# Kernel tuning notes

Hardware: AMD Instinct MI355X
Metric: run time of the kernel (lower is better)

Reference implementation:

```python
import jax, jax.numpy as jnp
import numpy as np

EPS = 1e-10
B, S, D, K = 8, 2048, 512, 1024
TEMP = 1.0  # quantizer temperature set to 1.0 in SQVAE.__init__


def _ln(x, g, b):
    m = x.mean(-1, keepdims=True)
    v = x.var(-1, keepdims=True)
    return (x - m) / jnp.sqrt(v + 1e-5) * g + b


def _mlp(x, w1, b1, g1, be1, w2, b2, g2, be2):
    # feed_forward: Linear -> ReLU -> LayerNorm, twice (MLPLayers=2)
    h = _ln(jax.nn.relu(x @ w1 + b1), g1, be1)
    return _ln(jax.nn.relu(h @ w2 + b2), g2, be2)


def setup_inputs() -> dict:
    key = jax.random.key(0)
    ks = jax.random.split(key, 20)
    W = 0.04  # small init scale to keep distances / softmax well-conditioned
    p = lambda k, sh, s=1.0: jax.random.normal(k, sh, dtype=jnp.float32) * s
    return {
        'x': p(ks[0], (B, S, D)),
        'gumbel_u': jax.random.uniform(ks[1], (B * S, K), dtype=jnp.float32),
        'enc_w1': p(ks[2], (D, D), W), 'enc_b1': jnp.zeros(D, jnp.float32),
        'enc_g1': jnp.ones(D, jnp.float32), 'enc_be1': jnp.zeros(D, jnp.float32),
        'enc_w2': p(ks[3], (D, D), W), 'enc_b2': jnp.zeros(D, jnp.float32),
        'enc_g2': jnp.ones(D, jnp.float32), 'enc_be2': jnp.zeros(D, jnp.float32),
        'dec_w1': p(ks[4], (D, D), W), 'dec_b1': jnp.zeros(D, jnp.float32),
        'dec_g1': jnp.ones(D, jnp.float32), 'dec_be1': jnp.zeros(D, jnp.float32),
        'dec_w2': p(ks[5], (D, D), W), 'dec_b2': jnp.zeros(D, jnp.float32),
        'dec_g2': jnp.ones(D, jnp.float32), 'dec_be2': jnp.zeros(D, jnp.float32),
        'codebook': p(ks[6], (K, D)),
        'log_param_q': jnp.zeros((), jnp.float32),
    }


def reference(x, gumbel_u, enc_w1, enc_b1, enc_g1, enc_be1, enc_w2, enc_b2, enc_g2, enc_be2,
              dec_w1, dec_b1, dec_g1, dec_be1, dec_w2, dec_b2, dec_g2, dec_be2,
              codebook, log_param_q):
    bs, seq, d = x.shape
    z = _mlp(x, enc_w1, enc_b1, enc_g1, enc_be1, enc_w2, enc_b2, enc_g2, enc_be2)
    # gaussian_1: log_var_q = 0 -> var_q = exp(log_param_q_scalar)
    var_q = jnp.exp(log_param_q)
    w = 0.5 / jnp.clip(var_q, 1e-10)  # 0.5 * precision_q (scalar)
    zf = z.reshape(-1, d)  # [N, D]
    # cdist^2 style distance, scaled by weight -> logits [N, K]
    dist = w * (jnp.sum(zf * zf, axis=1, keepdims=True)
                + jnp.sum(codebook * codebook, axis=1)
                - 2.0 * zf @ codebook.T)
    logit = -dist
    logp = jax.nn.log_softmax(logit, axis=-1)
    probs = jnp.exp(logp)
    # gumbel-softmax sample (train path), noise provided as uniform input
    g = -jnp.log(-jnp.log(gumbel_u + EPS) + EPS)
    encodings = jax.nn.softmax((logit + g) / TEMP, axis=-1)
    z_q = (encodings @ codebook).reshape(bs, seq, d)
    kld_discrete = jnp.sum(probs * logp) / bs
    kld_continuous = jnp.mean(jnp.sum((z - z_q) ** 2 * w, axis=(1, 2)))
    loss = kld_discrete + kld_continuous
    avg_probs = jnp.mean(jax.lax.stop_gradient(probs), axis=0)
    perplexity = jnp.exp(-jnp.sum(avg_probs * jnp.log(avg_probs + 1e-7)))
    x_rec = _mlp(z_q, dec_w1, dec_b1, dec_g1, dec_be1, dec_w2, dec_b2, dec_g2, dec_be2)
    return x_rec, loss, perplexity
```

## Files before the change

### kernel.cpp

```cpp
#include <hip/hip_runtime.h>
#include <math.h>

#define NROWS 16384
#define DIM   512
#define KCODE 1024

typedef __attribute__((ext_vector_type(8))) __bf16 bf16x8;
typedef __attribute__((ext_vector_type(4))) float f32x4;

__device__ __forceinline__ float wave_reduce_sum(float v) {
  #pragma unroll
  for (int m = 1; m < 64; m <<= 1) v += __shfl_xor(v, m, 64);
  return v;
}
__device__ __forceinline__ float wave_reduce_max(float v) {
  #pragma unroll
  for (int m = 1; m < 64; m <<= 1) v = fmaxf(v, __shfl_xor(v, m, 64));
  return v;
}
__device__ __forceinline__ unsigned short f2bf(float f) {
  union { float f; unsigned u; } v; v.f = f;
  unsigned r = v.u + 0x7FFFu + ((v.u >> 16) & 1u);
  return (unsigned short)(r >> 16);
}
__device__ __forceinline__ float bf2f(unsigned short h) {
  union { unsigned u; float f; } v; v.u = ((unsigned)h) << 16;
  return v.f;
}
__device__ __forceinline__ uint4 pack8(const float* x) {
  uint4 r;
  r.x = (unsigned)f2bf(x[0]) | ((unsigned)f2bf(x[1]) << 16);
  r.y = (unsigned)f2bf(x[2]) | ((unsigned)f2bf(x[3]) << 16);
  r.z = (unsigned)f2bf(x[4]) | ((unsigned)f2bf(x[5]) << 16);
  r.w = (unsigned)f2bf(x[6]) | ((unsigned)f2bf(x[7]) << 16);
  return r;
}

__device__ __forceinline__ void glds16(const void* g, void* lds) {
  __builtin_amdgcn_global_load_lds(
      (const __attribute__((address_space(1))) unsigned int*)g,
      (__attribute__((address_space(3))) unsigned int*)lds, 16, 0, 0);
}

__global__ __launch_bounds__(512, 2) void dist_fused(
    const unsigned short* __restrict__ zhp, const unsigned short* __restrict__ zlp,
    const unsigned short* __restrict__ cbh, const unsigned short* __restrict__ cbl,
    const float* __restrict__ znorm, const float* __restrict__ cnorm,
    const float* __restrict__ lpq, float* __restrict__ outf) {
  __shared__ char smem[131072];
  const int t = threadIdx.x;
  const int l = t & 63, w = t >> 6;
  const int wm = w >> 2, wn = w & 3;
  const int b = blockIdx.x;
  const int xcd = b & 7, j = b >> 3;
  const int m0 = (xcd * 8 + j / 4) * 256;
  const int n0 = (j % 4) * 256;

  f32x4 acc[8][4];
  #pragma unroll
  for (int i = 0; i < 8; ++i)
    #pragma unroll
    for (int jj = 0; jj < 4; ++jj) acc[i][jj] = (f32x4){0.f, 0.f, 0.f, 0.f};

  const int row = l & 15;
  const int kcol = (l >> 4) * 8;
  const size_t aLo = (size_t)(m0 + w * 16 + row) * 512 + kcol;
  const size_t aHi = aLo + (size_t)128 * 512;
  const size_t bLo = (size_t)(n0 + w * 16 + row) * 512 + kcol;
  const size_t bHi = bLo + (size_t)128 * 512;

  auto issue = [&](int s) {
    char* hb = smem + (s & 1) * 65536;
    const int kt = s * 32;
    glds16(zhp + aLo + kt, hb + w * 1024);
    glds16(zhp + aHi + kt, hb + (w + 8) * 1024);
    glds16(zlp + aLo + kt, hb + 16384 + w * 1024);
    glds16(zlp + aHi + kt, hb + 16384 + (w + 8) * 1024);
    glds16(cbh + bLo + kt, hb + 32768 + w * 1024);
    glds16(cbh + bHi + kt, hb + 32768 + (w + 8) * 1024);
    glds16(cbl + bLo + kt, hb + 49152 + w * 1024);
    glds16(cbl + bHi + kt, hb + 49152 + (w + 8) * 1024);
  };

  issue(0);
  #pragma unroll 1
  for (int s = 0; s < 16; ++s) {
    if (s + 1 < 16) {
      issue(s + 1);
      asm volatile("s_waitcnt vmcnt(8)" ::: "memory");
    } else {
      asm volatile("s_waitcnt vmcnt(0)" ::: "memory");
    }
    __builtin_amdgcn_s_barrier();
    const char* hb = smem + (s & 1) * 65536;
    bf16x8 af[8], bh[4], bl_[4];
    #pragma unroll
    for (int i = 0; i < 4; ++i) {
      bh[i]  = *(const bf16x8*)(hb + 32768 + (wn * 4 + i) * 1024 + l * 16);
      bl_[i] = *(const bf16x8*)(hb + 49152 + (wn * 4 + i) * 1024 + l * 16);
    }
    #pragma unroll
    for (int i = 0; i < 8; ++i)
      af[i] = *(const bf16x8*)(hb + (wm * 8 + i) * 1024 + l * 16);
    #pragma unroll
    for (int mi = 0; mi < 8; ++mi)
      #pragma unroll
      for (int ni = 0; ni < 4; ++ni) {
        acc[mi][ni] = __builtin_amdgcn_mfma_f32_16x16x32_bf16(af[mi], bh[ni], acc[mi][ni], 0, 0, 0);
        acc[mi][ni] = __builtin_amdgcn_mfma_f32_16x16x32_bf16(af[mi], bl_[ni], acc[mi][ni], 0, 0, 0);
      }
    #pragma unroll
    for (int i = 0; i < 8; ++i)
      af[i] = *(const bf16x8*)(hb + 16384 + (wm * 8 + i) * 1024 + l * 16);
    #pragma unroll
    for (int mi = 0; mi < 8; ++mi)
      #pragma unroll
      for (int ni = 0; ni < 4; ++ni)
        acc[mi][ni] = __builtin_amdgcn_mfma_f32_16x16x32_bf16(af[mi], bh[ni], acc[mi][ni], 0, 0, 0);
    __builtin_amdgcn_s_barrier();
  }

  float* slab = (float*)(smem + w * 4352);
  const int q = l >> 4, c16 = l & 15;
  const int c4 = (l & 15) * 4;
  const float wq = 0.5f / fmaxf(expf(lpq[0]), 1e-10f);

  #pragma unroll
  for (int mi = 0; mi < 8; ++mi) {
    __syncthreads();
    #pragma unroll
    for (int ni = 0; ni < 4; ++ni)
      #pragma unroll
      for (int r = 0; r < 4; ++r)
        slab[(q * 4 + r) * 68 + ni * 16 + c16] = acc[mi][ni][r];
    __syncthreads();
    #pragma unroll
    for (int pp = 0; pp < 4; ++pp) {
      const int rw = pp * 4 + q;
      const float4 v4 = *(const float4*)&slab[rw * 68 + c4];
      const int m = m0 + wm * 128 + mi * 16 + rw;
      const int nc = n0 + wn * 64 + c4;
      const float zn = znorm[m];
      const float4 cn = *(const float4*)&cnorm[nc];
      float4 o;
      o.x = -wq * (zn + cn.x - 2.f * v4.x);
      o.y = -wq * (zn + cn.y - 2.f * v4.y);
      o.z = -wq * (zn + cn.z - 2.f * v4.z);
      o.w = -wq * (zn + cn.w - 2.f * v4.w);
      *(float4*)&outf[(size_t)m * KCODE + nc] = o;
    }
  }
}

template <int NPASS, int EPI, int K, int N, int LDA, int MROWS>
__global__ __launch_bounds__(512, 2) void gemm256(
    const unsigned short* A0, const unsigned short* A1, const unsigned short* A2,
    const unsigned short* B0, const unsigned short* B1, const unsigned short* B2,
    const float* __restrict__ znorm, const float* __restrict__ cnorm,
    const float* __restrict__ lpq,
    const unsigned short* __restrict__ zh, const unsigned short* __restrict__ zl,
    float* __restrict__ kldc,
    unsigned short* __restrict__ outb, float* __restrict__ outf) {
  __shared__ char smem[65536];
  const int t = threadIdx.x;
  const int l = t & 63, w = t >> 6;
  const int wm = w >> 2, wn = w & 3;
  const int NTN = N / 256;
  const int b = blockIdx.x;
  const int xcd = b & 7, j = b >> 3;
  const int MT_PER_XCD = (MROWS / 256) / 8;
  const int m0 = (xcd * MT_PER_XCD + j / NTN) * 256;
  const int n0 = (j % NTN) * 256;

  f32x4 acc[8][4];
  #pragma unroll
  for (int i = 0; i < 8; ++i)
    #pragma unroll
    for (int jj = 0; jj < 4; ++jj) acc[i][jj] = (f32x4){0.f, 0.f, 0.f, 0.f};

  const int row_lo = w * 16 + (l & 15);
  const int row_hi = (w + 8) * 16 + (l & 15);
  const int kcol = (l >> 4) * 8;
  const int dA0 = w * 1024;
  const int dA1 = (w + 8) * 1024;
  const int dB0 = 16384 + w * 1024;
  const int dB1 = 16384 + (w + 8) * 1024;

  const size_t oA0 = (size_t)(m0 + row_lo) * LDA + kcol;
  const size_t oA1 = (size_t)(m0 + row_hi) * LDA + kcol;
  const size_t oB0 = (size_t)(n0 + row_lo) * K + kcol;
  const size_t oB1 = (size_t)(n0 + row_hi) * K + kcol;

  constexpr int SPP = K / 32;
  constexpr int NSTEP = NPASS * SPP;

  auto issue = [&](int ss) {
    const int p = (NPASS == 1) ? 0 : (ss / SPP);
    const int kt = (ss % SPP) * 32;
    const unsigned short* A = (p == 0) ? A0 : (p == 1) ? A1 : A2;
    const unsigned short* B = (p == 0) ? B0 : (p == 1) ? B1 : B2;
    char* hb = smem + (ss & 1) * 32768;
    glds16(A + oA0 + kt, hb + dA0);
    glds16(A + oA1 + kt, hb + dA1);
    glds16(B + oB0 + kt, hb + dB0);
    glds16(B + oB1 + kt, hb + dB1);
  };

  issue(0);
  #pragma unroll 1
  for (int s = 0; s < NSTEP; ++s) {
    if (s + 1 < NSTEP) {
      issue(s + 1);
      asm volatile("s_waitcnt vmcnt(4)" ::: "memory");
    } else {
      asm volatile("s_waitcnt vmcnt(0)" ::: "memory");
    }
    __builtin_amdgcn_s_barrier();
    const char* hb = smem + (s & 1) * 32768;
    bf16x8 af[8], bfr[4];
    #pragma unroll
    for (int i = 0; i < 4; ++i)
      bfr[i] = *(const bf16x8*)(hb + 16384 + (wn * 4 + i) * 1024 + l * 16);
    #pragma unroll
    for (int i = 0; i < 8; ++i)
      af[i] = *(const bf16x8*)(hb + (wm * 8 + i) * 1024 + l * 16);
    #pragma unroll
    for (int mi = 0; mi < 8; ++mi)
      #pragma unroll
      for (int ni = 0; ni < 4; ++ni)
        acc[mi][ni] = __builtin_amdgcn_mfma_f32_16x16x32_bf16(af[mi], bfr[ni], acc[mi][ni], 0, 0, 0);
    __builtin_amdgcn_s_barrier();
  }

  float* slab = (float*)(smem + w * 4352);
  const int q = l >> 4, c16 = l & 15;
  const int c4 = (l & 15) * 4;
  const float wq = 0.5f / fmaxf(expf(lpq[0]), 1e-10f);
  float local = 0.f;

  #pragma unroll
  for (int mi = 0; mi < 8; ++mi) {
    __syncthreads();
    #pragma unroll
    for (int ni = 0; ni < 4; ++ni)
      #pragma unroll
      for (int r = 0; r < 4; ++r)
        slab[(q * 4 + r) * 68 + ni * 16 + c16] = acc[mi][ni][r];
    __syncthreads();
    #pragma unroll
    for (int pp = 0; pp < 4; ++pp) {
      const int rw = pp * 4 + q;
      const float4 v4 = *(const float4*)&slab[rw * 68 + c4];
      float v[4] = {v4.x, v4.y, v4.z, v4.w};
      const int m = m0 + wm * 128 + mi * 16 + rw;
      const int nc = n0 + wn * 64 + c4;
      if (EPI == 1) {
        const float zn = znorm[m];
        const float4 cn = *(const float4*)&cnorm[nc];
        float4 o;
        o.x = -wq * (zn + cn.x - 2.f * v[0]);
        o.y = -wq * (zn + cn.y - 2.f * v[1]);
        o.z = -wq * (zn + cn.z - 2.f * v[2]);
        o.w = -wq * (zn + cn.w - 2.f * v[3]);
        *(float4*)&outf[(size_t)m * N + nc] = o;
      } else {
        const uint2 h2 = *(const uint2*)&zh[(size_t)m * N + nc];
        const uint2 l2 = *(const uint2*)&zl[(size_t)m * N + nc];
        const float z0 = bf2f((unsigned short)(h2.x & 0xFFFF)) + bf2f((unsigned short)(l2.x & 0xFFFF));
        const float z1 = bf2f((unsigned short)(h2.x >> 16))    + bf2f((unsigned short)(l2.x >> 16));
        const float z2 = bf2f((unsigned short)(h2.y & 0xFFFF)) + bf2f((unsigned short)(l2.y & 0xFFFF));
        const float z3 = bf2f((unsigned short)(h2.y >> 16))    + bf2f((unsigned short)(l2.y >> 16));
        const float d0 = z0 - v[0], d1 = z1 - v[1], d2 = z2 - v[2], d3 = z3 - v[3];
        local += d0 * d0 + d1 * d1 + d2 * d2 + d3 * d3;
        uint2 st;
        st.x = (unsigned)f2bf(v[0]) | ((unsigned)f2bf(v[1]) << 16);
        st.y = (unsigned)f2bf(v[2]) | ((unsigned)f2bf(v[3]) << 16);
        *(uint2*)&outb[(size_t)m * N + nc] = st;
      }
    }
  }
  if (EPI == 2) {
    local = wave_reduce_sum(local) * wq;
    if (l == 0) atomicAdd(kldc, local);
  }
}

template <int NPASS, int EPI, int K, int N, int LDA>
__global__ __launch_bounds__(256) void gemm_bt(
    const unsigned short* A0, const unsigned short* A1, const unsigned short* A2,
    const unsigned short* B0, const unsigned short* B1, const unsigned short* B2,
    const float* __restrict__ bias,
    const float* __restrict__ znorm, const float* __restrict__ cnorm,
    const float* __restrict__ lpq,
    const unsigned short* __restrict__ zh, const unsigned short* __restrict__ zl,
    float* __restrict__ kldc,
    unsigned short* __restrict__ outb, float* __restrict__ outf) {
  __shared__ char smem[32768];
  const int t = threadIdx.x;
  const int l = t & 63, w = t >> 6;
  const int wm = w >> 1, wn = w & 1;
  const int NTN = N / 128;
  const int b = blockIdx.x;
  const int xcd = b & 7;
  const int j = b >> 3;
  const int m0 = (xcd * 16 + j / NTN) * 128;
  const int n0 = (j % NTN) * 128;

  f32x4 acc[4][4];
  #pragma unroll
  for (int i = 0; i < 4; ++i)
    #pragma unroll
    for (int jj = 0; jj < 4; ++jj) acc[i][jj] = (f32x4){0.f, 0.f, 0.f, 0.f};

  const int row_lo = w * 16 + (l & 15);
  const int row_hi = (w + 4) * 16 + (l & 15);
  const int kcol = (l >> 4) * 8;
  const int dA0 = w * 1024;
  const int dA1 = (w + 4) * 1024;
  const int dB0 = 8192 + w * 1024;
  const int dB1 = 8192 + (w + 4) * 1024;

  const size_t oA0 = (size_t)(m0 + row_lo) * LDA + kcol;
  const size_t oA1 = (size_t)(m0 + row_hi) * LDA + kcol;
  const size_t oB0 = (size_t)(n0 + row_lo) * K + kcol;
  const size_t oB1 = (size_t)(n0 + row_hi) * K + kcol;

  constexpr int SPP = K / 32;
  constexpr int NSTEP = NPASS * SPP;

  auto issue = [&](int ss) {
    const int p = (NPASS == 1) ? 0 : (ss / SPP);
    const int kt = (ss % SPP) * 32;
    const unsigned short* A = (p == 0) ? A0 : (p == 1) ? A1 : A2;
    const unsigned short* B = (p == 0) ? B0 : (p == 1) ? B1 : B2;
    char* hb = smem + (ss & 1) * 16384;
    glds16(A + oA0 + kt, hb + dA0);
    glds16(A + oA1 + kt, hb + dA1);
    glds16(B + oB0 + kt, hb + dB0);
    glds16(B + oB1 + kt, hb + dB1);
  };

  issue(0);
  #pragma unroll 1
  for (int s = 0; s < NSTEP; ++s) {
    if (s + 1 < NSTEP) {
      issue(s + 1);
      asm volatile("s_waitcnt vmcnt(4)" ::: "memory");
    } else {
      asm volatile("s_waitcnt vmcnt(0)" ::: "memory");
    }
    __builtin_amdgcn_s_barrier();
    const char* hb = smem + (s & 1) * 16384;
    bf16x8 af[4], bfr[4];
    #pragma unroll
    for (int i = 0; i < 4; ++i) {
      af[i]  = *(const bf16x8*)(hb + (wm * 4 + i) * 1024 + l * 16);
      bfr[i] = *(const bf16x8*)(hb + 8192 + (wn * 4 + i) * 1024 + l * 16);
    }
    #pragma unroll
    for (int mi = 0; mi < 4; ++mi)
      #pragma unroll
      for (int ni = 0; ni < 4; ++ni)
        acc[mi][ni] = __builtin_amdgcn_mfma_f32_16x16x32_bf16(af[mi], bfr[ni], acc[mi][ni], 0, 0, 0);
    __builtin_amdgcn_s_barrier();
  }

  float* slab = (float*)(smem + w * 4352);
  const int q = l >> 4, c16 = l & 15;
  const int c4 = (l & 15) * 4;
  const float wq = (EPI >= 1) ? 0.5f / fmaxf(expf(lpq[0]), 1e-10f) : 0.f;
  float local = 0.f;

  #pragma unroll
  for (int mi = 0; mi < 4; ++mi) {
    __syncthreads();
    #pragma unroll
    for (int ni = 0; ni < 4; ++ni)
      #pragma unroll
      for (int r = 0; r < 4; ++r)
        slab[(q * 4 + r) * 68 + ni * 16 + c16] = acc[mi][ni][r];
    __syncthreads();
    #pragma unroll
    for (int pp = 0; pp < 4; ++pp) {
      const int rw = pp * 4 + q;
      const float4 v4 = *(const float4*)&slab[rw * 68 + c4];
      float v[4] = {v4.x, v4.y, v4.z, v4.w};
      const int m = m0 + wm * 64 + mi * 16 + rw;
      const int nc = n0 + wn * 64 + c4;
      if (EPI == 0) {
        const float4 b4 = *(const float4*)&bias[nc];
        v[0] = fmaxf(v[0] + b4.x, 0.f);
        v[1] = fmaxf(v[1] + b4.y, 0.f);
        v[2] = fmaxf(v[2] + b4.z, 0.f);
        v[3] = fmaxf(v[3] + b4.w, 0.f);
        uint2 st;
        st.x = (unsigned)f2bf(v[0]) | ((unsigned)f2bf(v[1]) << 16);
        st.y = (unsigned)f2bf(v[2]) | ((unsigned)f2bf(v[3]) << 16);
        *(uint2*)&outb[(size_t)m * N + nc] = st;
      } else if (EPI == 1) {
        const float zn = znorm[m];
        const float4 cn = *(const float4*)&cnorm[nc];
        float4 o;
        o.x = -wq * (zn + cn.x - 2.f * v[0]);
        o.y = -wq * (zn + cn.y - 2.f * v[1]);
        o.z = -wq * (zn + cn.z - 2.f * v[2]);
        o.w = -wq * (zn + cn.w - 2.f * v[3]);
        *(float4*)&outf[(size_t)m * N + nc] = o;
      } else {
        const uint2 h2 = *(const uint2*)&zh[(size_t)m * N + nc];
        const uint2 l2 = *(const uint2*)&zl[(size_t)m * N + nc];
        const float z0 = bf2f((unsigned short)(h2.x & 0xFFFF)) + bf2f((unsigned short)(l2.x & 0xFFFF));
        const float z1 = bf2f((unsigned short)(h2.x >> 16))    + bf2f((unsigned short)(l2.x >> 16));
        const float z2 = bf2f((unsigned short)(h2.y & 0xFFFF)) + bf2f((unsigned short)(l2.y & 0xFFFF));
        const float z3 = bf2f((unsigned short)(h2.y >> 16))    + bf2f((unsigned short)(l2.y >> 16));
        const float d0 = z0 - v[0], d1 = z1 - v[1], d2 = z2 - v[2], d3 = z3 - v[3];
        local += d0 * d0 + d1 * d1 + d2 * d2 + d3 * d3;
        uint2 st;
        st.x = (unsigned)f2bf(v[0]) | ((unsigned)f2bf(v[1]) << 16);
        st.y = (unsigned)f2bf(v[2]) | ((unsigned)f2bf(v[3]) << 16);
        *(uint2*)&outb[(size_t)m * N + nc] = st;
      }
    }
  }
  if (EPI == 2) {
    local = wave_reduce_sum(local) * wq;
    if (l == 0) atomicAdd(kldc, local);
  }
}

template <int MODE>
__global__ __launch_bounds__(256) void ln_rows(
    const unsigned short* __restrict__ X, const float* __restrict__ g,
    const float* __restrict__ be, unsigned short* __restrict__ Y,
    unsigned short* __restrict__ Yl, float* __restrict__ znorm,
    float* __restrict__ Yf) {
  const int l = threadIdx.x & 63, wv = threadIdx.x >> 6;
  float gv[8], bv[8];
  {
    const float4 a = *(const float4*)&g[l * 8];
    const float4 b = *(const float4*)&g[l * 8 + 4];
    gv[0] = a.x; gv[1] = a.y; gv[2] = a.z; gv[3] = a.w;
    gv[4] = b.x; gv[5] = b.y; gv[6] = b.z; gv[7] = b.w;
    const float4 c = *(const float4*)&be[l * 8];
    const float4 d = *(const float4*)&be[l * 8 + 4];
    bv[0] = c.x; bv[1] = c.y; bv[2] = c.z; bv[3] = c.w;
    bv[4] = d.x; bv[5] = d.y; bv[6] = d.z; bv[7] = d.w;
  }
  const int row0 = blockIdx.x * 32 + wv * 8;
  for (int rr = 0; rr < 8; ++rr) {
    const int row = row0 + rr;
    const uint4 raw = *(const uint4*)&X[(size_t)row * 512 + l * 8];
    float v[8];
    const unsigned rw[4] = {raw.x, raw.y, raw.z, raw.w};
    #pragma unroll
    for (int i = 0; i < 4; ++i) {
      v[2 * i]     = bf2f((unsigned short)(rw[i] & 0xFFFF));
      v[2 * i + 1] = bf2f((unsigned short)(rw[i] >> 16));
    }
    float s = 0.f, ss = 0.f;
    #pragma unroll
    for (int i = 0; i < 8; ++i) { s += v[i]; ss += v[i] * v[i]; }
    #pragma unroll
    for (int m = 1; m < 64; m <<= 1) {
      s += __shfl_xor(s, m, 64);
      ss += __shfl_xor(ss, m, 64);
    }
    const float mean = s * (1.f / 512.f);
    const float var = ss * (1.f / 512.f) - mean * mean;
    const float rstd = rsqrtf(var + 1e-5f);
    float y[8];
    #pragma unroll
    for (int i = 0; i < 8; ++i) y[i] = (v[i] - mean) * rstd * gv[i] + bv[i];
    if (MODE == 0) {
      *(uint4*)&Y[(size_t)row * 512 + l * 8] = pack8(y);
    } else if (MODE == 1) {
      float lo[8], ns = 0.f;
      unsigned short hx[8];
      #pragma unroll
      for (int i = 0; i < 8; ++i) {
        hx[i] = f2bf(y[i]);
        lo[i] = y[i] - bf2f(hx[i]);
        ns += y[i] * y[i];
      }
      uint4 hv;
      hv.x = (unsigned)hx[0] | ((unsigned)hx[1] << 16);
      hv.y = (unsigned)hx[2] | ((unsigned)hx[3] << 16);
      hv.z = (unsigned)hx[4] | ((unsigned)hx[5] << 16);
      hv.w = (unsigned)hx[6] | ((unsigned)hx[7] << 16);
      *(uint4*)&Y[(size_t)row * 512 + l * 8] = hv;
      *(uint4*)&Yl[(size_t)row * 512 + l * 8] = pack8(lo);
      ns = wave_reduce_sum(ns);
      if (l == 0) znorm[row] = ns;
    } else {
      float4 o0, o1;
      o0.x = y[0]; o0.y = y[1]; o0.z = y[2]; o0.w = y[3];
      o1.x = y[4]; o1.y = y[5]; o1.z = y[6]; o1.w = y[7];
      *(float4*)&Yf[(size_t)row * 512 + l * 8] = o0;
      *(float4*)&Yf[(size_t)row * 512 + l * 8 + 4] = o1;
    }
  }
}

__global__ __launch_bounds__(256) void convert_f32_bf16(
    const float* __restrict__ X, unsigned short* __restrict__ Y) {
  const size_t i = ((size_t)blockIdx.x * 256 + threadIdx.x) * 8;
  const float4 a = *(const float4*)&X[i];
  const float4 b = *(const float4*)&X[i + 4];
  float v[8] = {a.x, a.y, a.z, a.w, b.x, b.y, b.z, b.w};
  *(uint4*)&Y[i] = pack8(v);
}

__global__ __launch_bounds__(256) void prep_cb(
    const float* __restrict__ CB, unsigned short* __restrict__ H,
    unsigned short* __restrict__ L, float* __restrict__ cnorm) {
  const int wv = threadIdx.x >> 6, l = threadIdx.x & 63;
  const int r = blockIdx.x * 4 + wv;
  const float* row = &CB[(size_t)r * 512 + l * 8];
  const float4 a = *(const float4*)row;
  const float4 b = *(const float4*)(row + 4);
  float x[8] = {a.x, a.y, a.z, a.w, b.x, b.y, b.z, b.w};
  float s = 0.f, lo[8];
  unsigned short hi[8];
  #pragma unroll
  for (int i = 0; i < 8; ++i) {
    s += x[i] * x[i];
    hi[i] = f2bf(x[i]);
    lo[i] = x[i] - bf2f(hi[i]);
  }
  uint4 hv;
  hv.x = (unsigned)hi[0] | ((unsigned)hi[1] << 16);
  hv.y = (unsigned)hi[2] | ((unsigned)hi[3] << 16);
  hv.z = (unsigned)hi[4] | ((unsigned)hi[5] << 16);
  hv.w = (unsigned)hi[6] | ((unsigned)hi[7] << 16);
  *(uint4*)&H[(size_t)r * 512 + l * 8] = hv;
  *(uint4*)&L[(size_t)r * 512 + l * 8] = pack8(lo);
  s = wave_reduce_sum(s);
  if (l == 0) cnorm[r] = s;
}

__global__ __launch_bounds__(256) void transpose_f32_bf16(
    const float* __restrict__ in, unsigned short* __restrict__ out, int R, int C) {
  __shared__ float tile[32][33];
  const int ntc = C >> 5;
  const int c0 = (blockIdx.x % ntc) * 32, r0 = (blockIdx.x / ntc) * 32;
  const int tx = threadIdx.x & 31, ty = threadIdx.x >> 5;
  #pragma unroll
  for (int i = 0; i < 4; ++i)
    tile[ty + 8 * i][tx] = in[(size_t)(r0 + ty + 8 * i) * C + c0 + tx];
  __syncthreads();
  #pragma unroll
  for (int i = 0; i < 4; ++i)
    out[(size_t)(c0 + ty + 8 * i) * R + r0 + tx] = f2bf(tile[tx][ty + 8 * i]);
}

__global__ __launch_bounds__(256) void softmax_gumbel(
    const float* logits, const float* __restrict__ U, unsigned short* E,
    float* __restrict__ colsum, float* __restrict__ kldd_acc) {
  __shared__ float cs[1024];
  __shared__ float kd[4];
  const int t = threadIdx.x;
  const int wv = t >> 6, l = t & 63;
  #pragma unroll
  for (int i = 0; i < 4; ++i) cs[t + 256 * i] = 0.f;
  __syncthreads();
  float psum[16];
  #pragma unroll
  for (int i = 0; i < 16; ++i) psum[i] = 0.f;
  float kldd = 0.f;
  const int nbase = blockIdx.x * 16 + wv * 4;

  for (int it = 0; it < 4; ++it) {
    const int row = nbase + it;
    const size_t off = (size_t)row * KCODE + 4 * l;
    float v[16];
    #pragma unroll
    for (int jj = 0; jj < 4; ++jj) {
      const float4 t4 = *(const float4*)&logits[off + 256 * jj];
      v[4 * jj + 0] = t4.x; v[4 * jj + 1] = t4.y; v[4 * jj + 2] = t4.z; v[4 * jj + 3] = t4.w;
    }
    float m = v[0];
    #pragma unroll
    for (int i = 1; i < 16; ++i) m = fmaxf(m, v[i]);
    m = wave_reduce_max(m);
    float se = 0.f;
    #pragma unroll
    for (int i = 0; i < 16; ++i) se += expf(v[i] - m);
    se = wave_reduce_sum(se);
    const float lz = logf(se);
    float pl = 0.f;
    #pragma unroll
    for (int i = 0; i < 16; ++i) {
      const float lp = v[i] - m - lz;
      const float p = expf(lp);
      psum[i] += p;
      pl += p * lp;
    }
    kldd += pl;
    float y[16];
    #pragma unroll
    for (int jj = 0; jj < 4; ++jj) {
      const float4 t4 = *(const float4*)&U[off + 256 * jj];
      y[4 * jj + 0] = v[4 * jj + 0] - logf(-logf(t4.x + 1e-10f) + 1e-10f);
      y[4 * jj + 1] = v[4 * jj + 1] - logf(-logf(t4.y + 1e-10f) + 1e-10f);
      y[4 * jj + 2] = v[4 * jj + 2] - logf(-logf(t4.z + 1e-10f) + 1e-10f);
      y[4 * jj + 3] = v[4 * jj + 3] - logf(-logf(t4.w + 1e-10f) + 1e-10f);
    }
    float m2 = y[0];
    #pragma unroll
    for (int i = 1; i < 16; ++i) m2 = fmaxf(m2, y[i]);
    m2 = wave_reduce_max(m2);
    float s2 = 0.f;
    #pragma unroll
    for (int i = 0; i < 16; ++i) s2 += expf(y[i] - m2);
    s2 = wave_reduce_sum(s2);
    const float inv = 1.f / s2;
    #pragma unroll
    for (int jj = 0; jj < 4; ++jj) {
      ushort4 e;
      e.x = f2bf(expf(y[4 * jj + 0] - m2) * inv);
      e.y = f2bf(expf(y[4 * jj + 1] - m2) * inv);
      e.z = f2bf(expf(y[4 * jj + 2] - m2) * inv);
      e.w = f2bf(expf(y[4 * jj + 3] - m2) * inv);
      *(ushort4*)&E[(size_t)row * 2048 + 4 * l + 256 * jj] = e;
    }
  }
  #pragma unroll
  for (int jj = 0; jj < 4; ++jj)
    #pragma unroll
    for (int c = 0; c < 4; ++c)
      atomicAdd(&cs[256 * jj + 4 * l + c], psum[4 * jj + c]);
  kldd = wave_reduce_sum(kldd);
  if (l == 0) kd[wv] = kldd;
  __syncthreads();
  #pragma unroll
  for (int i = 0; i < 4; ++i) {
    const float vv = cs[t + 256 * i];
    if (vv != 0.f) atomicAdd(&colsum[t + 256 * i], vv);
  }
  if (t == 0) atomicAdd(kldd_acc, kd[0] + kd[1] + kd[2] + kd[3]);
}

__global__ __launch_bounds__(256) void finalize(
    const float* __restrict__ colsum, const float* __restrict__ scal,
    float* __restrict__ out) {
  const int t = threadIdx.x;
  float ent = 0.f;
  #pragma unroll
  for (int jj = 0; jj < 4; ++jj) {
    const float a = colsum[t + 256 * jj] * (1.f / 16384.f);
    ent += a * logf(a + 1e-7f);
  }
  ent = wave_reduce_sum(ent);
  __shared__ float red[4];
  if ((t & 63) == 0) red[t >> 6] = ent;
  __syncthreads();
  if (t == 0) {
    const float tot = red[0] + red[1] + red[2] + red[3];
    out[0] = (scal[0] + scal[1]) * (1.f / 8.f);
    out[1] = expf(-tot);
  }
}

extern "C" void kernel_launch(void* const* d_in, const int* in_sizes, int n_in,
                              void* d_out, int out_size, void* d_ws, size_t ws_size,
                              hipStream_t stream) {
  const float* x      = (const float*)d_in[0];
  const float* gu     = (const float*)d_in[1];
  const float* enc_w1 = (const float*)d_in[2];
  const float* enc_b1 = (const float*)d_in[3];
  const float* enc_g1 = (const float*)d_in[4];
  const float* enc_e1 = (const float*)d_in[5];
  const float* enc_w2 = (const float*)d_in[6];
  const float* enc_b2 = (const float*)d_in[7];
  const float* enc_g2 = (const float*)d_in[8];
  const float* enc_e2 = (const float*)d_in[9];
  const float* dec_w1 = (const float*)d_in[10];
  const float* dec_b1 = (const float*)d_in[11];
  const float* dec_g1 = (const float*)d_in[12];
  const float* dec_e1 = (const float*)d_in[13];
  const float* dec_w2 = (const float*)d_in[14];
  const float* dec_b2 = (const float*)d_in[15];
  const float* dec_g2 = (const float*)d_in[16];
  const float* dec_e2 = (const float*)d_in[17];
  const float* cb     = (const float*)d_in[18];
  const float* lpq    = (const float*)d_in[19];
  float* out = (float*)d_out;
  char* wsb = (char*)d_ws;

  float*          logits = (float*)(wsb + 0);
  unsigned short* Eb     = (unsigned short*)(wsb + 0);
  unsigned short* t1     = (unsigned short*)(wsb + 67108864);
  unsigned short* xb     = (unsigned short*)(wsb + 83886080);
  unsigned short* zh     = xb;
  unsigned short* hq     = (unsigned short*)(wsb + 100663296);
  unsigned short* zl     = (unsigned short*)(wsb + 117440512);
  unsigned short* wt0    = (unsigned short*)(wsb + 134217728);
  unsigned short* wt1    = wt0 + 262144;
  unsigned short* wt2    = wt1 + 262144;
  unsigned short* wt3    = wt2 + 262144;
  unsigned short* cbh    = (unsigned short*)(wsb + 136314880);
  unsigned short* cbl    = (unsigned short*)(wsb + 137363456);
  unsigned short* cbT    = (unsigned short*)(wsb + 138412032);
  float*          znorm  = (float*)(wsb + 139460608);
  float*          cnorm  = (float*)(wsb + 139526144);
  float*          colsum = (float*)(wsb + 139530240);
  float*          scal   = (float*)(wsb + 139534336);

  hipMemsetAsync(colsum, 0, 4096 + 16, stream);

  convert_f32_bf16<<<4096, 256, 0, stream>>>(x, xb);
  prep_cb<<<256, 256, 0, stream>>>(cb, cbh, cbl, cnorm);
  transpose_f32_bf16<<<256, 256, 0, stream>>>(enc_w1, wt0, 512, 512);
  transpose_f32_bf16<<<256, 256, 0, stream>>>(enc_w2, wt1, 512, 512);
  transpose_f32_bf16<<<256, 256, 0, stream>>>(dec_w1, wt2, 512, 512);
  transpose_f32_bf16<<<256, 256, 0, stream>>>(dec_w2, wt3, 512, 512);
  transpose_f32_bf16<<<512, 256, 0, stream>>>(cb, cbT, 1024, 512);

  gemm_bt<1, 0, 512, 512, 512><<<512, 256, 0, stream>>>(
      xb, nullptr, nullptr, wt0, nullptr, nullptr, enc_b1,
      nullptr, nullptr, nullptr, nullptr, nullptr, nullptr, t1, nullptr);
  ln_rows<0><<<512, 256, 0, stream>>>(t1, enc_g1, enc_e1, hq, nullptr, nullptr, nullptr);
  gemm_bt<1, 0, 512, 512, 512><<<512, 256, 0, stream>>>(
      hq, nullptr, nullptr, wt1, nullptr, nullptr, enc_b2,
      nullptr, nullptr, nullptr, nullptr, nullptr, nullptr, t1, nullptr);
  ln_rows<1><<<512, 256, 0, stream>>>(t1, enc_g2, enc_e2, zh, zl, znorm, nullptr);
  dist_fused<<<256, 512, 0, stream>>>(
      zh, zl, cbh, cbl, znorm, cnorm, lpq, logits);
  softmax_gumbel<<<1024, 256, 0, stream>>>(logits, gu, Eb, colsum, &scal[0]);
  gemm256<1, 2, 1024, 512, 2048, 16384><<<128, 512, 0, stream>>>(
      Eb, nullptr, nullptr, cbT, nullptr, nullptr,
      nullptr, nullptr, lpq, zh, zl, &scal[1], hq, nullptr);
  gemm_bt<1, 0, 512, 512, 512><<<512, 256, 0, stream>>>(
      hq, nullptr, nullptr, wt2, nullptr, nullptr, dec_b1,
      nullptr, nullptr, nullptr, nullptr, nullptr, nullptr, t1, nullptr);
  ln_rows<0><<<512, 256, 0, stream>>>(t1, dec_g1, dec_e1, zl, nullptr, nullptr, nullptr);
  gemm_bt<1, 0, 512, 512, 512><<<512, 256, 0, stream>>>(
      zl, nullptr, nullptr, wt3, nullptr, nullptr, dec_b2,
      nullptr, nullptr, nullptr, nullptr, nullptr, nullptr, t1, nullptr);
  ln_rows<2><<<512, 256, 0, stream>>>(t1, dec_g2, dec_e2, nullptr, nullptr, nullptr, out);
  finalize<<<1, 256, 0, stream>>>(colsum, scal, out + 8388608);
}
```

Baseline: 463.1 us.

## Load B fragments directly from global into registers, halve LDS staging

```diff
diff --git a/kernel.cpp b/kernel.cpp
--- a/kernel.cpp
+++ b/kernel.cpp
@@ -47,7 +47,7 @@
     const unsigned short* __restrict__ cbh, const unsigned short* __restrict__ cbl,
     const float* __restrict__ znorm, const float* __restrict__ cnorm,
     const float* __restrict__ lpq, float* __restrict__ outf) {
-  __shared__ char smem[131072];
+  __shared__ char smem[65536];
   const int t = threadIdx.x;
   const int l = t & 63, w = t >> 6;
   const int wm = w >> 2, wn = w & 3;
@@ -66,39 +66,38 @@
   const int kcol = (l >> 4) * 8;
   const size_t aLo = (size_t)(m0 + w * 16 + row) * 512 + kcol;
   const size_t aHi = aLo + (size_t)128 * 512;
-  const size_t bLo = (size_t)(n0 + w * 16 + row) * 512 + kcol;
-  const size_t bHi = bLo + (size_t)128 * 512;
+
+  const unsigned short* __restrict__ cbhB = cbh + (size_t)(n0 + row) * 512 + kcol;
+  const unsigned short* __restrict__ cblB = cbl + (size_t)(n0 + row) * 512 + kcol;
 
   auto issue = [&](int s) {
-    char* hb = smem + (s & 1) * 65536;
+    char* hb = smem + (s & 1) * 32768;
     const int kt = s * 32;
     glds16(zhp + aLo + kt, hb + w * 1024);
     glds16(zhp + aHi + kt, hb + (w + 8) * 1024);
     glds16(zlp + aLo + kt, hb + 16384 + w * 1024);
     glds16(zlp + aHi + kt, hb + 16384 + (w + 8) * 1024);
-    glds16(cbh + bLo + kt, hb + 32768 + w * 1024);
-    glds16(cbh + bHi + kt, hb + 32768 + (w + 8) * 1024);
-    glds16(cbl + bLo + kt, hb + 49152 + w * 1024);
-    glds16(cbl + bHi + kt, hb + 49152 + (w + 8) * 1024);
   };
 
   issue(0);
   #pragma unroll 1
   for (int s = 0; s < 16; ++s) {
+    const int kt2 = s * 32;
+    bf16x8 bh[4], blf[4];
+    #pragma unroll
+    for (int i = 0; i < 4; ++i) {
+      bh[i]  = *(const bf16x8*)(cbhB + (size_t)(wn * 4 + i) * 8192 + kt2);
+      blf[i] = *(const bf16x8*)(cblB + (size_t)(wn * 4 + i) * 8192 + kt2);
+    }
     if (s + 1 < 16) {
       issue(s + 1);
+      asm volatile("s_waitcnt vmcnt(12)" ::: "memory");
+    } else {
       asm volatile("s_waitcnt vmcnt(8)" ::: "memory");
-    } else {
-      asm volatile("s_waitcnt vmcnt(0)" ::: "memory");
     }
     __builtin_amdgcn_s_barrier();
-    const char* hb = smem + (s & 1) * 65536;
-    bf16x8 af[8], bh[4], bl_[4];
-    #pragma unroll
-    for (int i = 0; i < 4; ++i) {
-      bh[i]  = *(const bf16x8*)(hb + 32768 + (wn * 4 + i) * 1024 + l * 16);
-      bl_[i] = *(const bf16x8*)(hb + 49152 + (wn * 4 + i) * 1024 + l * 16);
-    }
+    const char* hb = smem + (s & 1) * 32768;
+    bf16x8 af[8];
     #pragma unroll
     for (int i = 0; i < 8; ++i)
       af[i] = *(const bf16x8*)(hb + (wm * 8 + i) * 1024 + l * 16);
@@ -107,7 +106,7 @@
       #pragma unroll
       for (int ni = 0; ni < 4; ++ni) {
         acc[mi][ni] = __builtin_amdgcn_mfma_f32_16x16x32_bf16(af[mi], bh[ni], acc[mi][ni], 0, 0, 0);
-        acc[mi][ni] = __builtin_amdgcn_mfma_f32_16x16x32_bf16(af[mi], bl_[ni], acc[mi][ni], 0, 0, 0);
+        acc[mi][ni] = __builtin_amdgcn_mfma_f32_16x16x32_bf16(af[mi], blf[ni], acc[mi][ni], 0, 0, 0);
       }
     #pragma unroll
     for (int i = 0; i < 8; ++i)
@@ -152,16 +151,15 @@
   }
 }
 
-template <int NPASS, int EPI, int K, int N, int LDA, int MROWS>
+template <int EPI, int K, int N, int LDA, int MROWS>
 __global__ __launch_bounds__(512, 2) void gemm256(
-    const unsigned short* A0, const unsigned short* A1, const unsigned short* A2,
-    const unsigned short* B0, const unsigned short* B1, const unsigned short* B2,
+    const unsigned short* A0, const unsigned short* B0,
     const float* __restrict__ znorm, const float* __restrict__ cnorm,
     const float* __restrict__ lpq,
     const unsigned short* __restrict__ zh, const unsigned short* __restrict__ zl,
     float* __restrict__ kldc,
     unsigned short* __restrict__ outb, float* __restrict__ outf) {
-  __shared__ char smem[65536];
+  __shared__ char smem[34816];
   const int t = threadIdx.x;
   const int l = t & 63, w = t >> 6;
   const int wm = w >> 2, wn = w & 3;
@@ -178,49 +176,38 @@
     #pragma unroll
     for (int jj = 0; jj < 4; ++jj) acc[i][jj] = (f32x4){0.f, 0.f, 0.f, 0.f};
 
-  const int row_lo = w * 16 + (l & 15);
-  const int row_hi = (w + 8) * 16 + (l & 15);
+  const int row = l & 15;
   const int kcol = (l >> 4) * 8;
-  const int dA0 = w * 1024;
-  const int dA1 = (w + 8) * 1024;
-  const int dB0 = 16384 + w * 1024;
-  const int dB1 = 16384 + (w + 8) * 1024;
-
-  const size_t oA0 = (size_t)(m0 + row_lo) * LDA + kcol;
-  const size_t oA1 = (size_t)(m0 + row_hi) * LDA + kcol;
-  const size_t oB0 = (size_t)(n0 + row_lo) * K + kcol;
-  const size_t oB1 = (size_t)(n0 + row_hi) * K + kcol;
-
-  constexpr int SPP = K / 32;
-  constexpr int NSTEP = NPASS * SPP;
+  const size_t oA0 = (size_t)(m0 + w * 16 + row) * LDA + kcol;
+  const size_t oA1 = oA0 + (size_t)128 * LDA;
+  const unsigned short* __restrict__ Bb = B0 + (size_t)(n0 + row) * K + kcol;
+
+  constexpr int NSTEP = K / 32;
 
   auto issue = [&](int ss) {
-    const int p = (NPASS == 1) ? 0 : (ss / SPP);
-    const int kt = (ss % SPP) * 32;
-    const unsigned short* A = (p == 0) ? A0 : (p == 1) ? A1 : A2;
-    const unsigned short* B = (p == 0) ? B0 : (p == 1) ? B1 : B2;
-    char* hb = smem + (ss & 1) * 32768;
-    glds16(A + oA0 + kt, hb + dA0);
-    glds16(A + oA1 + kt, hb + dA1);
-    glds16(B + oB0 + kt, hb + dB0);
-    glds16(B + oB1 + kt, hb + dB1);
+    char* hb = smem + (ss & 1) * 16384;
+    const int kt = ss * 32;
+    glds16(A0 + oA0 + kt, hb + w * 1024);
+    glds16(A0 + oA1 + kt, hb + (w + 8) * 1024);
   };
 
   issue(0);
   #pragma unroll 1
   for (int s = 0; s < NSTEP; ++s) {
+    const int kt2 = s * 32;
+    bf16x8 bfr[4];
+    #pragma unroll
+    for (int i = 0; i < 4; ++i)
+      bfr[i] = *(const bf16x8*)(Bb + (size_t)(wn * 4 + i) * 16 * K + kt2);
     if (s + 1 < NSTEP) {
       issue(s + 1);
+      asm volatile("s_waitcnt vmcnt(6)" ::: "memory");
+    } else {
       asm volatile("s_waitcnt vmcnt(4)" ::: "memory");
-    } else {
-      asm volatile("s_waitcnt vmcnt(0)" ::: "memory");
     }
     __builtin_amdgcn_s_barrier();
-    const char* hb = smem + (s & 1) * 32768;
-    bf16x8 af[8], bfr[4];
-    #pragma unroll
-    for (int i = 0; i < 4; ++i)
-      bfr[i] = *(const bf16x8*)(hb + 16384 + (wn * 4 + i) * 1024 + l * 16);
+    const char* hb = smem + (s & 1) * 16384;
+    bf16x8 af[8];
     #pragma unroll
     for (int i = 0; i < 8; ++i)
       af[i] = *(const bf16x8*)(hb + (wm * 8 + i) * 1024 + l * 16);
@@ -285,17 +272,12 @@
   }
 }
 
-template <int NPASS, int EPI, int K, int N, int LDA>
+template <int EPI, int K, int N, int LDA>
 __global__ __launch_bounds__(256) void gemm_bt(
-    const unsigned short* A0, const unsigned short* A1, const unsigned short* A2,
-    const unsigned short* B0, const unsigned short* B1, const unsigned short* B2,
+    const unsigned short* A0, const unsigned short* B0,
     const float* __restrict__ bias,
-    const float* __restrict__ znorm, const float* __restrict__ cnorm,
-    const float* __restrict__ lpq,
-    const unsigned short* __restrict__ zh, const unsigned short* __restrict__ zl,
-    float* __restrict__ kldc,
-    unsigned short* __restrict__ outb, float* __restrict__ outf) {
-  __shared__ char smem[32768];
+    unsigned short* __restrict__ outb) {
+  __shared__ char smem[17408];
   const int t = threadIdx.x;
   const int l = t & 63, w = t >> 6;
   const int wm = w >> 1, wn = w & 1;
@@ -312,51 +294,41 @@
     #pragma unroll
     for (int jj = 0; jj < 4; ++jj) acc[i][jj] = (f32x4){0.f, 0.f, 0.f, 0.f};
 
-  const int row_lo = w * 16 + (l & 15);
-  const int row_hi = (w + 4) * 16 + (l & 15);
+  const int row = l & 15;
   const int kcol = (l >> 4) * 8;
-  const int dA0 = w * 1024;
-  const int dA1 = (w + 4) * 1024;
-  const int dB0 = 8192 + w * 1024;
-  const int dB1 = 8192 + (w + 4) * 1024;
-
-  const size_t oA0 = (size_t)(m0 + row_lo) * LDA + kcol;
-  const size_t oA1 = (size_t)(m0 + row_hi) * LDA + kcol;
-  const size_t oB0 = (size_t)(n0 + row_lo) * K + kcol;
-  const size_t oB1 = (size_t)(n0 + row_hi) * K + kcol;
-
-  constexpr int SPP = K / 32;
-  constexpr int NSTEP = NPASS * SPP;
+  const size_t oA0 = (size_t)(m0 + w * 16 + row) * LDA + kcol;
+  const size_t oA1 = oA0 + (size_t)64 * LDA;
+  const unsigned short* __restrict__ Bb = B0 + (size_t)(n0 + row) * K + kcol;
+
+  constexpr int NSTEP = K / 32;
 
   auto issue = [&](int ss) {
-    const int p = (NPASS == 1) ? 0 : (ss / SPP);
-    const int kt = (ss % SPP) * 32;
-    const unsigned short* A = (p == 0) ? A0 : (p == 1) ? A1 : A2;
-    const unsigned short* B = (p == 0) ? B0 : (p == 1) ? B1 : B2;
-    char* hb = smem + (ss & 1) * 16384;
-    glds16(A + oA0 + kt, hb + dA0);
-    glds16(A + oA1 + kt, hb + dA1);
-    glds16(B + oB0 + kt, hb + dB0);
-    glds16(B + oB1 + kt, hb + dB1);
+    char* hb = smem + (ss & 1) * 8192;
+    const int kt = ss * 32;
+    glds16(A0 + oA0 + kt, hb + w * 1024);
+    glds16(A0 + oA1 + kt, hb + (w + 4) * 1024);
   };
 
   issue(0);
   #pragma unroll 1
   for (int s = 0; s < NSTEP; ++s) {
+    const int kt2 = s * 32;
+    bf16x8 bfr[4];
+    #pragma unroll
+    for (int i = 0; i < 4; ++i)
+      bfr[i] = *(const bf16x8*)(Bb + (size_t)(wn * 4 + i) * 16 * K + kt2);
     if (s + 1 < NSTEP) {
       issue(s + 1);
+      asm volatile("s_waitcnt vmcnt(6)" ::: "memory");
+    } else {
       asm volatile("s_waitcnt vmcnt(4)" ::: "memory");
-    } else {
-      asm volatile("s_waitcnt vmcnt(0)" ::: "memory");
     }
     __builtin_amdgcn_s_barrier();
-    const char* hb = smem + (s & 1) * 16384;
-    bf16x8 af[4], bfr[4];
-    #pragma unroll
-    for (int i = 0; i < 4; ++i) {
-      af[i]  = *(const bf16x8*)(hb + (wm * 4 + i) * 1024 + l * 16);
-      bfr[i] = *(const bf16x8*)(hb + 8192 + (wn * 4 + i) * 1024 + l * 16);
-    }
+    const char* hb = smem + (s & 1) * 8192;
+    bf16x8 af[4];
+    #pragma unroll
+    for (int i = 0; i < 4; ++i)
+      af[i] = *(const bf16x8*)(hb + (wm * 4 + i) * 1024 + l * 16);
     #pragma unroll
     for (int mi = 0; mi < 4; ++mi)
       #pragma unroll
@@ -368,8 +340,6 @@
   float* slab = (float*)(smem + w * 4352);
   const int q = l >> 4, c16 = l & 15;
   const int c4 = (l & 15) * 4;
-  const float wq = (EPI >= 1) ? 0.5f / fmaxf(expf(lpq[0]), 1e-10f) : 0.f;
-  float local = 0.f;
 
   #pragma unroll
   for (int mi = 0; mi < 4; ++mi) {
@@ -387,44 +357,16 @@
       float v[4] = {v4.x, v4.y, v4.z, v4.w};
       const int m = m0 + wm * 64 + mi * 16 + rw;
       const int nc = n0 + wn * 64 + c4;
-      if (EPI == 0) {
-        const float4 b4 = *(const float4*)&bias[nc];
-        v[0] = fmaxf(v[0] + b4.x, 0.f);
-        v[1] = fmaxf(v[1] + b4.y, 0.f);
-        v[2] = fmaxf(v[2] + b4.z, 0.f);
-        v[3] = fmaxf(v[3] + b4.w, 0.f);
-        uint2 st;
-        st.x = (unsigned)f2bf(v[0]) | ((unsigned)f2bf(v[1]) << 16);
-        st.y = (unsigned)f2bf(v[2]) | ((unsigned)f2bf(v[3]) << 16);
-        *(uint2*)&outb[(size_t)m * N + nc] = st;
-      } else if (EPI == 1) {
-        const float zn = znorm[m];
-        const float4 cn = *(const float4*)&cnorm[nc];
-        float4 o;
-        o.x = -wq * (zn + cn.x - 2.f * v[0]);
-        o.y = -wq * (zn + cn.y - 2.f * v[1]);
-        o.z = -wq * (zn + cn.z - 2.f * v[2]);
-        o.w = -wq * (zn + cn.w - 2.f * v[3]);
-        *(float4*)&outf[(size_t)m * N + nc] = o;
-      } else {
-        const uint2 h2 = *(const uint2*)&zh[(size_t)m * N + nc];
-        const uint2 l2 = *(const uint2*)&zl[(size_t)m * N + nc];
-        const float z0 = bf2f((unsigned short)(h2.x & 0xFFFF)) + bf2f((unsigned short)(l2.x & 0xFFFF));
-        const float z1 = bf2f((unsigned short)(h2.x >> 16))    + bf2f((unsigned short)(l2.x >> 16));
-        const float z2 = bf2f((unsigned short)(h2.y & 0xFFFF)) + bf2f((unsigned short)(l2.y & 0xFFFF));
-        const float z3 = bf2f((unsigned short)(h2.y >> 16))    + bf2f((unsigned short)(l2.y >> 16));
-        const float d0 = z0 - v[0], d1 = z1 - v[1], d2 = z2 - v[2], d3 = z3 - v[3];
-        local += d0 * d0 + d1 * d1 + d2 * d2 + d3 * d3;
-        uint2 st;
-        st.x = (unsigned)f2bf(v[0]) | ((unsigned)f2bf(v[1]) << 16);
-        st.y = (unsigned)f2bf(v[2]) | ((unsigned)f2bf(v[3]) << 16);
-        *(uint2*)&outb[(size_t)m * N + nc] = st;
-      }
-    }
-  }
-  if (EPI == 2) {
-    local = wave_reduce_sum(local) * wq;
-    if (l == 0) atomicAdd(kldc, local);
+      const float4 b4 = *(const float4*)&bias[nc];
+      v[0] = fmaxf(v[0] + b4.x, 0.f);
+      v[1] = fmaxf(v[1] + b4.y, 0.f);
+      v[2] = fmaxf(v[2] + b4.z, 0.f);
+      v[3] = fmaxf(v[3] + b4.w, 0.f);
+      uint2 st;
+      st.x = (unsigned)f2bf(v[0]) | ((unsigned)f2bf(v[1]) << 16);
+      st.y = (unsigned)f2bf(v[2]) | ((unsigned)f2bf(v[3]) << 16);
+      *(uint2*)&outb[(size_t)m * N + nc] = st;
+    }
   }
 }
 
@@ -582,46 +524,46 @@
     #pragma unroll
     for (int i = 1; i < 16; ++i) m = fmaxf(m, v[i]);
     m = wave_reduce_max(m);
-    float se = 0.f;
-    #pragma unroll
-    for (int i = 0; i < 16; ++i) se += expf(v[i] - m);
+    float e[16], se = 0.f;
+    #pragma unroll
+    for (int i = 0; i < 16; ++i) { e[i] = __expf(v[i] - m); se += e[i]; }
     se = wave_reduce_sum(se);
-    const float lz = logf(se);
+    const float lz = __logf(se);
+    const float inv_se = 1.f / se;
     float pl = 0.f;
     #pragma unroll
     for (int i = 0; i < 16; ++i) {
-      const float lp = v[i] - m - lz;
-      const float p = expf(lp);
+      const float p = e[i] * inv_se;
       psum[i] += p;
-      pl += p * lp;
+      pl += p * (v[i] - m - lz);
     }
     kldd += pl;
     float y[16];
     #pragma unroll
     for (int jj = 0; jj < 4; ++jj) {
       const float4 t4 = *(const float4*)&U[off + 256 * jj];
-      y[4 * jj + 0] = v[4 * jj + 0] - logf(-logf(t4.x + 1e-10f) + 1e-10f);
-      y[4 * jj + 1] = v[4 * jj + 1] - logf(-logf(t4.y + 1e-10f) + 1e-10f);
-      y[4 * jj + 2] = v[4 * jj + 2] - logf(-logf(t4.z + 1e-10f) + 1e-10f);
-      y[4 * jj + 3] = v[4 * jj + 3] - logf(-logf(t4.w + 1e-10f) + 1e-10f);
+      y[4 * jj + 0] = v[4 * jj + 0] - __logf(-__logf(t4.x + 1e-10f) + 1e-10f);
+      y[4 * jj + 1] = v[4 * jj + 1] - __logf(-__logf(t4.y + 1e-10f) + 1e-10f);
+      y[4 * jj + 2] = v[4 * jj + 2] - __logf(-__logf(t4.z + 1e-10f) + 1e-10f);
+      y[4 * jj + 3] = v[4 * jj + 3] - __logf(-__logf(t4.w + 1e-10f) + 1e-10f);
     }
     float m2 = y[0];
     #pragma unroll
     for (int i = 1; i < 16; ++i) m2 = fmaxf(m2, y[i]);
     m2 = wave_reduce_max(m2);
-    float s2 = 0.f;
-    #pragma unroll
-    for (int i = 0; i < 16; ++i) s2 += expf(y[i] - m2);
+    float ey[16], s2 = 0.f;
+    #pragma unroll
+    for (int i = 0; i < 16; ++i) { ey[i] = __expf(y[i] - m2); s2 += ey[i]; }
     s2 = wave_reduce_sum(s2);
     const float inv = 1.f / s2;
     #pragma unroll
     for (int jj = 0; jj < 4; ++jj) {
-      ushort4 e;
-      e.x = f2bf(expf(y[4 * jj + 0] - m2) * inv);
-      e.y = f2bf(expf(y[4 * jj + 1] - m2) * inv);
-      e.z = f2bf(expf(y[4 * jj + 2] - m2) * inv);
-      e.w = f2bf(expf(y[4 * jj + 3] - m2) * inv);
-      *(ushort4*)&E[(size_t)row * 2048 + 4 * l + 256 * jj] = e;
+      ushort4 e4;
+      e4.x = f2bf(ey[4 * jj + 0] * inv);
+      e4.y = f2bf(ey[4 * jj + 1] * inv);
+      e4.z = f2bf(ey[4 * jj + 2] * inv);
+      e4.w = f2bf(ey[4 * jj + 3] * inv);
+      *(ushort4*)&E[(size_t)row * 2048 + 4 * l + 256 * jj] = e4;
     }
   }
   #pragma unroll
@@ -716,27 +658,18 @@
   transpose_f32_bf16<<<256, 256, 0, stream>>>(dec_w2, wt3, 512, 512);
   transpose_f32_bf16<<<512, 256, 0, stream>>>(cb, cbT, 1024, 512);
 
-  gemm_bt<1, 0, 512, 512, 512><<<512, 256, 0, stream>>>(
-      xb, nullptr, nullptr, wt0, nullptr, nullptr, enc_b1,
-      nullptr, nullptr, nullptr, nullptr, nullptr, nullptr, t1, nullptr);
+  gemm_bt<0, 512, 512, 512><<<512, 256, 0, stream>>>(xb, wt0, enc_b1, t1);
   ln_rows<0><<<512, 256, 0, stream>>>(t1, enc_g1, enc_e1, hq, nullptr, nullptr, nullptr);
-  gemm_bt<1, 0, 512, 512, 512><<<512, 256, 0, stream>>>(
-      hq, nullptr, nullptr, wt1, nullptr, nullptr, enc_b2,
-      nullptr, nullptr, nullptr, nullptr, nullptr, nullptr, t1, nullptr);
+  gemm_bt<0, 512, 512, 512><<<512, 256, 0, stream>>>(hq, wt1, enc_b2, t1);
   ln_rows<1><<<512, 256, 0, stream>>>(t1, enc_g2, enc_e2, zh, zl, znorm, nullptr);
   dist_fused<<<256, 512, 0, stream>>>(
       zh, zl, cbh, cbl, znorm, cnorm, lpq, logits);
   softmax_gumbel<<<1024, 256, 0, stream>>>(logits, gu, Eb, colsum, &scal[0]);
-  gemm256<1, 2, 1024, 512, 2048, 16384><<<128, 512, 0, stream>>>(
-      Eb, nullptr, nullptr, cbT, nullptr, nullptr,
-      nullptr, nullptr, lpq, zh, zl, &scal[1], hq, nullptr);
-  gemm_bt<1, 0, 512, 512, 512><<<512, 256, 0, stream>>>(
-      hq, nullptr, nullptr, wt2, nullptr, nullptr, dec_b1,
-      nullptr, nullptr, nullptr, nullptr, nullptr, nullptr, t1, nullptr);
+  gemm256<2, 1024, 512, 2048, 16384><<<128, 512, 0, stream>>>(
+      Eb, cbT, nullptr, nullptr, lpq, zh, zl, &scal[1], hq, nullptr);
+  gemm_bt<0, 512, 512, 512><<<512, 256, 0, stream>>>(hq, wt2, dec_b1, t1);
   ln_rows<0><<<512, 256, 0, stream>>>(t1, dec_g1, dec_e1, zl, nullptr, nullptr, nullptr);
-  gemm_bt<1, 0, 512, 512, 512><<<512, 256, 0, stream>>>(
-      zl, nullptr, nullptr, wt3, nullptr, nullptr, dec_b2,
-      nullptr, nullptr, nullptr, nullptr, nullptr, nullptr, t1, nullptr);
+  gemm_bt<0, 512, 512, 512><<<512, 256, 0, stream>>>(zl, wt3, dec_b2, t1);
   ln_rows<2><<<512, 256, 0, stream>>>(t1, dec_g2, dec_e2, nullptr, nullptr, nullptr, out);
   finalize<<<1, 256, 0, stream>>>(colsum, scal, out + 8388608);
 }
```

Measured after the change: 524.1 us. 1.13x slower.
